# Kernel tuning notes

Measured on AMD Instinct MI355X. Metric: run time of the kernel, lower is better.

Reference implementation:

```python
import jax, jax.numpy as jnp
import numpy as np

DIM = 256
HEADS = 4


def setup_inputs() -> dict:
    key = jax.random.key(0)
    k1, k2, k3, k4, k5 = jax.random.split(key, 5)
    x = jax.random.normal(k1, (8, DIM, 128, 128), dtype=jnp.float32)
    s_in = 1.0 / np.sqrt(DIM)
    Wqkv = jax.random.normal(k2, (DIM, 3 * DIM), dtype=jnp.float32) * s_in
    bqkv = jax.random.normal(k3, (3 * DIM,), dtype=jnp.float32) * 0.02
    Wproj = jax.random.normal(k4, (DIM, DIM), dtype=jnp.float32) * s_in
    bproj = jax.random.normal(k5, (DIM,), dtype=jnp.float32) * 0.02
    return {"x": x, "Wqkv": Wqkv, "bqkv": bqkv, "Wproj": Wproj, "bproj": bproj}


def reference(x, Wqkv, bqkv, Wproj, bproj):
    b, c, h, w = x.shape
    hd = c // HEADS  # head dim
    scale = hd ** -0.5
    # axis='h': (b c h w) -> (b*w, h, c)
    x_r = jnp.transpose(x, (0, 3, 2, 1)).reshape(b * w, h, c)
    qkv = x_r @ Wqkv + bqkv                              # [B, S, 3c]
    qkv = qkv.reshape(b * w, h, 3, HEADS, hd)
    qkv = jnp.transpose(qkv, (2, 0, 3, 1, 4))            # [3, B, H, S, d]
    q, k, v = qkv[0], qkv[1], qkv[2]
    attn = jax.nn.softmax(jnp.einsum('bhqd,bhkd->bhqk', q, k) * scale, axis=-1)
    out = jnp.einsum('bhqk,bhkd->bhqd', attn, v)         # [B, H, S, d]
    out = jnp.transpose(out, (0, 2, 1, 3)).reshape(b * w, h, c)
    out = out @ Wproj + bproj
    # (b*w, h, c) -> (b, c, h, w)
    out = out.reshape(b, w, h, c)
    return jnp.transpose(out, (0, 3, 2, 1))
```

## Files before the change

kernel.cpp:

```cpp
#include <hip/hip_runtime.h>


typedef _Float16 h4 __attribute__((ext_vector_type(4)));
typedef _Float16 h8 __attribute__((ext_vector_type(8)));
typedef float f4 __attribute__((ext_vector_type(4)));
typedef unsigned int u4 __attribute__((ext_vector_type(4)));

#define MFMA32(a, b, c) __builtin_amdgcn_mfma_f32_16x16x32_f16((a), (b), (c), 0, 0, 0)

__device__ __forceinline__ void gll16(const _Float16* g, _Float16* l) {
  __builtin_amdgcn_global_load_lds(
      (const __attribute__((address_space(1))) void*)g,
      (__attribute__((address_space(3))) void*)l, 16, 0, 0);
}

__global__ __launch_bounds__(256) void prep_w(const float* __restrict__ Wqkv,
                                              const float* __restrict__ Wproj,
                                              _Float16* __restrict__ wqt,
                                              _Float16* __restrict__ wpt) {
  int i = blockIdx.x * 256 + threadIdx.x;
  if (i < 768 * 256) {
    int f = i >> 8, c = i & 255;
    wqt[i] = (_Float16)Wqkv[c * 768 + f];
  } else {
    int j = i - 768 * 256;
    int f = j >> 8, c = j & 255;
    wpt[j] = (_Float16)Wproj[c * 256 + f];
  }
}

__global__ __launch_bounds__(256, 4) void k1f(const float* __restrict__ x,
                                              const _Float16* __restrict__ wqt,
                                              const float* __restrict__ bqkv,
                                              _Float16* __restrict__ qkv,
                                              int b_base, int nb) {
  const int wg = blockIdx.x;
  const int xcd = wg & 7, seq = wg >> 3;
  const int id = xcd * (nb * 32) + seq;
  const int hb = id & 127;
  const int rest = id >> 7;
  const int wh = rest & 1, bl = rest >> 1;
  const int b = b_base + bl;
  const int w0 = wh * 64;

  const int tid = threadIdx.x;
  const int lane = tid & 63, wv = tid >> 6;
  const int g = lane >> 4, l16 = lane & 15;
  const int wr = wv >> 1, wc = wv & 1;

  __shared__ __align__(16) char smem[34816];
  _Float16* sXT = (_Float16*)smem;
  _Float16* sA = (_Float16*)smem;
  _Float16* sO = (_Float16*)(smem + 16384);

  {
    const int j0 = tid & 7, r8 = tid >> 3;
#pragma unroll
    for (int p = 0; p < 8; ++p) {
      const int c = p * 32 + r8;
      const float* src = x + (((long)b * 256 + c) * 128 + hb) * 128 + w0;
      f4 v0 = *(const f4*)(src + j0 * 4);
      f4 v1 = *(const f4*)(src + (j0 + 8) * 4);
#pragma unroll
      for (int i = 0; i < 4; ++i) {
        sXT[(j0 * 4 + i) * 264 + c] = (_Float16)v0[i];
        sXT[((j0 + 8) * 4 + i) * 264 + c] = (_Float16)v1[i];
      }
    }
  }
  __syncthreads();

  h8 bfr[4][2][2];
#pragma unroll
  for (int kc = 0; kc < 4; ++kc)
#pragma unroll
    for (int ks = 0; ks < 2; ++ks)
#pragma unroll
      for (int nt = 0; nt < 2; ++nt) {
        const int t = wc * 32 + nt * 16 + l16;
        bfr[kc][ks][nt] =
            *(const h8*)(sXT + t * 264 + kc * 64 + ks * 32 + 8 * g);
      }
  __syncthreads();

  const int r0 = wv * 32;
  const int rl = lane >> 3;
  const int chs = ((lane & 7) ^ rl) * 8;
  const int wl = tid >> 2, dc = tid & 3;
  const int kx = (l16 & 7) * 8;

  for (int ft = 0; ft < 6; ++ft) {
    const int f0 = ft * 128;
    f4 acc[4][2];
#pragma unroll
    for (int mt = 0; mt < 4; ++mt)
#pragma unroll
      for (int nt = 0; nt < 2; ++nt)
#pragma unroll
        for (int r = 0; r < 4; ++r) acc[mt][nt][r] = 0.f;

    for (int kc = 0; kc < 4; ++kc) {
#pragma unroll
      for (int i = 0; i < 4; ++i) {
        const int row = r0 + i * 8 + rl;
        gll16(wqt + (long)(f0 + row) * 256 + kc * 64 + chs, sA + (r0 + i * 8) * 64);
      }
      __syncthreads();
#pragma unroll
      for (int ks = 0; ks < 2; ++ks) {
        const int kk = (ks * 32 + 8 * g) ^ kx;
        h8 af[4];
#pragma unroll
        for (int mt = 0; mt < 4; ++mt)
          af[mt] = *(const h8*)(sA + (wr * 64 + mt * 16 + l16) * 64 + kk);
#pragma unroll
        for (int mt = 0; mt < 4; ++mt)
#pragma unroll
          for (int nt = 0; nt < 2; ++nt)
            acc[mt][nt] = MFMA32(af[mt], bfr[kc][ks][nt], acc[mt][nt]);
      }
      __syncthreads();
    }

#pragma unroll
    for (int mt = 0; mt < 4; ++mt) {
      f4 bb = *(const f4*)(bqkv + f0 + wr * 64 + mt * 16 + 4 * g);
#pragma unroll
      for (int nt = 0; nt < 2; ++nt) {
        const int tl = wc * 32 + nt * 16 + l16;
#pragma unroll
        for (int r = 0; r < 4; ++r)
          sO[tl * 136 + wr * 64 + mt * 16 + 4 * g + r] =
              (_Float16)(acc[mt][nt][r] + bb[r]);
      }
    }
    __syncthreads();
#pragma unroll
    for (int h2 = 0; h2 < 2; ++h2) {
      const int fh = f0 + h2 * 64;
      const int qi = fh >> 8, head = (fh >> 6) & 3;
      _Float16* dst = qkv + (((long)(qi * nb + bl) * 4 + head) * 128 + hb) * 8192 +
                      (w0 + wl) * 64 + dc * 16;
      const _Float16* s = sO + wl * 136 + h2 * 64 + dc * 16;
      *(u4*)dst = *(const u4*)s;
      *(u4*)(dst + 8) = *(const u4*)(s + 8);
    }
    __syncthreads();
  }
}

__global__ __launch_bounds__(256) void k2_attn(const _Float16* __restrict__ qkv,
                                               _Float16* __restrict__ attnout,
                                               int nb) {
  const int w = blockIdx.x, head = blockIdx.y, bl = blockIdx.z;
  const int tid = threadIdx.x;
  const int lane = tid & 63, wv = tid >> 6;
  const int g = lane >> 4, l16 = lane & 15;

  __shared__ __align__(16) char smem[(128 * 72 * 2 + 64 * 136) * 2];
  _Float16* sQ = (_Float16*)smem;
  _Float16* sK = sQ + 128 * 72;
  _Float16* sVT = sK + 128 * 72;
  _Float16* sP = sQ;
  _Float16* sO = sQ;

  const long base = (((long)bl * 4 + head) * 128) * 8192 + (long)w * 64;
  const long QS = (long)nb * 4 * 128 * 8192;
  const _Float16* qg = qkv + base;
  const _Float16* kg = qkv + base + QS;
  const _Float16* vg = qkv + base + 2 * QS;

#pragma unroll
  for (int i = 0; i < 4; ++i) {
    int u = tid + 256 * i;
    int hh = u >> 3, dq = u & 7;
    *(u4*)(sQ + hh * 72 + dq * 8) = *(const u4*)(qg + (long)hh * 8192 + dq * 8);
    *(u4*)(sK + hh * 72 + dq * 8) = *(const u4*)(kg + (long)hh * 8192 + dq * 8);
  }
  {
    const int hh = tid & 127, dcv = tid >> 7;
#pragma unroll
    for (int jj = 0; jj < 4; ++jj) {
      u4 vv = *(const u4*)(vg + (long)hh * 8192 + dcv * 32 + jj * 8);
      const _Float16* pe = (const _Float16*)&vv;
#pragma unroll
      for (int e = 0; e < 8; ++e)
        sVT[(dcv * 32 + jj * 8 + e) * 136 + hh] = pe[e];
    }
  }
  __syncthreads();

  f4 accS[8][2];
  for (int i = 0; i < 8; ++i)
    for (int jt = 0; jt < 2; ++jt)
      for (int r = 0; r < 4; ++r) accS[i][jt][r] = 0.f;
#pragma unroll
  for (int ks = 0; ks < 2; ++ks) {
    const int k = ks * 32 + 8 * g;
    h8 af[8], bf[2];
#pragma unroll
    for (int i = 0; i < 8; ++i)
      af[i] = *(const h8*)(sK + (i * 16 + l16) * 72 + k);
#pragma unroll
    for (int jt = 0; jt < 2; ++jt)
      bf[jt] = *(const h8*)(sQ + (wv * 32 + jt * 16 + l16) * 72 + k);
#pragma unroll
    for (int i = 0; i < 8; ++i)
#pragma unroll
      for (int jt = 0; jt < 2; ++jt)
        accS[i][jt] = MFMA32(af[i], bf[jt], accS[i][jt]);
  }

  float rinv[2];
#pragma unroll
  for (int jt = 0; jt < 2; ++jt) {
    float m = -1e30f;
    for (int i = 0; i < 8; ++i)
      for (int r = 0; r < 4; ++r) m = fmaxf(m, accS[i][jt][r]);
    m = fmaxf(m, __shfl_xor(m, 16));
    m = fmaxf(m, __shfl_xor(m, 32));
    float s = 0.f;
    for (int i = 0; i < 8; ++i)
      for (int r = 0; r < 4; ++r) {
        float p = __expf((accS[i][jt][r] - m) * 0.125f);
        accS[i][jt][r] = p;
        s += p;
      }
    s += __shfl_xor(s, 16);
    s += __shfl_xor(s, 32);
    rinv[jt] = 1.0f / s;
  }

  __syncthreads();
#pragma unroll
  for (int jt = 0; jt < 2; ++jt) {
    const int hq = wv * 32 + jt * 16 + l16;
#pragma unroll
    for (int i = 0; i < 8; ++i) {
      h4 pv;
      pv[0] = (_Float16)accS[i][jt][0];
      pv[1] = (_Float16)accS[i][jt][1];
      pv[2] = (_Float16)accS[i][jt][2];
      pv[3] = (_Float16)accS[i][jt][3];
      *(h4*)(sP + hq * 136 + i * 16 + 4 * g) = pv;
    }
  }
  __syncthreads();

  f4 accO[4][2];
  for (int mt = 0; mt < 4; ++mt)
    for (int jt = 0; jt < 2; ++jt)
      for (int r = 0; r < 4; ++r) accO[mt][jt][r] = 0.f;
#pragma unroll
  for (int i2 = 0; i2 < 4; ++i2) {
    const int k = i2 * 32 + 8 * g;
    h8 av[4], pb[2];
#pragma unroll
    for (int mt = 0; mt < 4; ++mt)
      av[mt] = *(const h8*)(sVT + (mt * 16 + l16) * 136 + k);
#pragma unroll
    for (int jt = 0; jt < 2; ++jt)
      pb[jt] = *(const h8*)(sP + (wv * 32 + jt * 16 + l16) * 136 + k);
#pragma unroll
    for (int mt = 0; mt < 4; ++mt)
#pragma unroll
      for (int jt = 0; jt < 2; ++jt)
        accO[mt][jt] = MFMA32(av[mt], pb[jt], accO[mt][jt]);
  }

  __syncthreads();
#pragma unroll
  for (int mt = 0; mt < 4; ++mt)
#pragma unroll
    for (int jt = 0; jt < 2; ++jt)
#pragma unroll
      for (int r = 0; r < 4; ++r)
        sO[(wv * 32 + jt * 16 + l16) * 72 + mt * 16 + 4 * g + r] =
            (_Float16)(accO[mt][jt][r] * rinv[jt]);
  __syncthreads();

  const int hh = tid >> 1, d0 = (tid & 1) * 32;
  const _Float16* s = sO + hh * 72 + d0;
  _Float16* dst = attnout + ((long)bl * 16384 + hh * 128 + w) * 256 + head * 64 + d0;
#pragma unroll
  for (int e = 0; e < 4; ++e)
    *(u4*)(dst + e * 8) = *(const u4*)(s + e * 8);
}

__global__ __launch_bounds__(256, 4) void k3_proj(const _Float16* __restrict__ attnout,
                                                  const _Float16* __restrict__ wpt,
                                                  const float* __restrict__ bproj,
                                                  float* __restrict__ out,
                                                  int b_base, int nb) {
  const int ct = blockIdx.x, tt = blockIdx.y, bl = blockIdx.z;
  const int b = b_base + bl;
  const int tid = threadIdx.x;
  const int lane = tid & 63, wv = tid >> 6;
  const int g = lane >> 4, l16 = lane & 15;
  const int wr = wv >> 1, wc = wv & 1;
  const int co0 = ct * 128;
  const long t0 = (long)tt * 128;

  __shared__ __align__(16) char smem[33792];
  _Float16* sA = (_Float16*)smem;
  _Float16* sB = sA + 128 * 64;
  float* sOut = (float*)smem;

  f4 acc[4][4];
#pragma unroll
  for (int mt = 0; mt < 4; ++mt)
#pragma unroll
    for (int nt = 0; nt < 4; ++nt)
#pragma unroll
      for (int r = 0; r < 4; ++r) acc[mt][nt][r] = 0.f;

  const _Float16* Ab = wpt + (long)co0 * 256;
  const _Float16* Bb = attnout + ((long)bl * 16384 + t0) * 256;
  const int r0 = wv * 32;
  const int rl = lane >> 3;
  const int chs = ((lane & 7) ^ rl) * 8;
  const int kx = (l16 & 7) * 8;

  for (int kc = 0; kc < 4; ++kc) {
    const int c0 = kc * 64;
#pragma unroll
    for (int i = 0; i < 4; ++i) {
      const int row = r0 + i * 8 + rl;
      gll16(Ab + (long)row * 256 + c0 + chs, sA + (r0 + i * 8) * 64);
      gll16(Bb + (long)row * 256 + c0 + chs, sB + (r0 + i * 8) * 64);
    }
    __syncthreads();
#pragma unroll
    for (int ks = 0; ks < 2; ++ks) {
      const int kk = (ks * 32 + 8 * g) ^ kx;
      h8 af[4], bf[4];
#pragma unroll
      for (int mt = 0; mt < 4; ++mt)
        af[mt] = *(const h8*)(sA + (wr * 64 + mt * 16 + l16) * 64 + kk);
#pragma unroll
      for (int nt = 0; nt < 4; ++nt)
        bf[nt] = *(const h8*)(sB + (wc * 64 + nt * 16 + l16) * 64 + kk);
#pragma unroll
      for (int mt = 0; mt < 4; ++mt)
#pragma unroll
        for (int nt = 0; nt < 4; ++nt)
          acc[mt][nt] = MFMA32(af[mt], bf[nt], acc[mt][nt]);
    }
    __syncthreads();
  }

#pragma unroll
  for (int h2 = 0; h2 < 2; ++h2) {
    if (h2) __syncthreads();
    if (wr == h2) {
#pragma unroll
      for (int mt = 0; mt < 4; ++mt) {
        f4 bb = *(const f4*)(bproj + co0 + h2 * 64 + mt * 16 + 4 * g);
#pragma unroll
        for (int nt = 0; nt < 4; ++nt)
#pragma unroll
          for (int r = 0; r < 4; ++r)
            sOut[(mt * 16 + 4 * g + r) * 132 + wc * 64 + nt * 16 + l16] =
                acc[mt][nt][r] + bb[r];
      }
    }
    __syncthreads();
    const int row = tid >> 2, seg = (tid & 3) * 32;
    const float* s = sOut + row * 132 + seg;
    float* dst = out + ((long)b * 256 + co0 + h2 * 64 + row) * 16384 + t0 + seg;
#pragma unroll
    for (int e = 0; e < 8; ++e)
      *(f4*)(dst + e * 4) = *(const f4*)(s + e * 4);
  }
}

extern "C" void kernel_launch(void* const* d_in, const int* in_sizes, int n_in,
                              void* d_out, int out_size, void* d_ws, size_t ws_size,
                              hipStream_t stream) {
  const float* x = (const float*)d_in[0];
  const float* Wqkv = (const float*)d_in[1];
  const float* bqkv = (const float*)d_in[2];
  const float* Wproj = (const float*)d_in[3];
  const float* bproj = (const float*)d_in[4];
  float* out = (float*)d_out;

  char* ws = (char*)d_ws;
  const long WQT = 393216L, WPT = 131072L;
  const long PER_B = 25165824L + 8388608L;
  long nb_l = ((long)ws_size - (WQT + WPT)) / PER_B;
  int nb = nb_l < 1 ? 1 : (nb_l > 8 ? 8 : (int)nb_l);

  _Float16* wqt = (_Float16*)ws;
  _Float16* wpt = (_Float16*)(ws + WQT);
  _Float16* qkv = (_Float16*)(ws + WQT + WPT);
  _Float16* attnout = (_Float16*)(ws + WQT + WPT + (long)nb * 25165824L);

  prep_w<<<1024, 256, 0, stream>>>(Wqkv, Wproj, wqt, wpt);

  for (int b0 = 0; b0 < 8; b0 += nb) {
    int nbv = (8 - b0 < nb) ? (8 - b0) : nb;
    k1f<<<nbv * 256, 256, 0, stream>>>(x, wqt, bqkv, qkv, b0, nbv);
    k2_attn<<<dim3(128, 4, nbv), 256, 0, stream>>>(qkv, attnout, nbv);
    k3_proj<<<dim3(2, 128, nbv), 256, 0, stream>>>(attnout, wpt, bproj, out, b0, nbv);
  }
}
```

Baseline: 244.2 us.

## Widen QKV projection tile to full 128-column row per block

Each k1f block now handles all 128 w-positions of one (batch, h) row instead of half, so the grid halves and every block does twice the work. The 128x256 weight slice for each feature tile is loaded into LDS once per tile with an XOR swizzle, replacing the four per-k-chunk loads and their barriers. Each wave now covers 128 features by 32 tokens, which reuses each loaded weight fragment across more tokens. The cost is twice the LDS, more accumulator registers and lower occupancy (launch bound 2 instead of 4), and a weight-load phase that no longer overlaps compute.

```diff
diff --git a/kernel.cpp b/kernel.cpp
--- a/kernel.cpp
+++ b/kernel.cpp
@@ -29,42 +29,39 @@
   }
 }
 
-__global__ __launch_bounds__(256, 4) void k1f(const float* __restrict__ x,
+__global__ __launch_bounds__(256, 2) void k1f(const float* __restrict__ x,
                                               const _Float16* __restrict__ wqt,
                                               const float* __restrict__ bqkv,
                                               _Float16* __restrict__ qkv,
                                               int b_base, int nb) {
   const int wg = blockIdx.x;
   const int xcd = wg & 7, seq = wg >> 3;
-  const int id = xcd * (nb * 32) + seq;
+  const int id = xcd * (nb * 16) + seq;
   const int hb = id & 127;
-  const int rest = id >> 7;
-  const int wh = rest & 1, bl = rest >> 1;
+  const int bl = id >> 7;
   const int b = b_base + bl;
-  const int w0 = wh * 64;
 
   const int tid = threadIdx.x;
   const int lane = tid & 63, wv = tid >> 6;
   const int g = lane >> 4, l16 = lane & 15;
-  const int wr = wv >> 1, wc = wv & 1;
-
-  __shared__ __align__(16) char smem[34816];
+
+  __shared__ __align__(16) char smem[67584];
   _Float16* sXT = (_Float16*)smem;
   _Float16* sA = (_Float16*)smem;
-  _Float16* sO = (_Float16*)(smem + 16384);
+  _Float16* sO = (_Float16*)smem;
 
   {
-    const int j0 = tid & 7, r8 = tid >> 3;
-#pragma unroll
-    for (int p = 0; p < 8; ++p) {
-      const int c = p * 32 + r8;
-      const float* src = x + (((long)b * 256 + c) * 128 + hb) * 128 + w0;
+    const int j0 = tid & 15, r16 = tid >> 4;
+#pragma unroll
+    for (int p = 0; p < 16; ++p) {
+      const int c = p * 16 + r16;
+      const float* src = x + (((long)b * 256 + c) * 128 + hb) * 128;
       f4 v0 = *(const f4*)(src + j0 * 4);
-      f4 v1 = *(const f4*)(src + (j0 + 8) * 4);
+      f4 v1 = *(const f4*)(src + (j0 + 16) * 4);
 #pragma unroll
       for (int i = 0; i < 4; ++i) {
         sXT[(j0 * 4 + i) * 264 + c] = (_Float16)v0[i];
-        sXT[((j0 + 8) * 4 + i) * 264 + c] = (_Float16)v1[i];
+        sXT[((j0 + 16) * 4 + i) * 264 + c] = (_Float16)v1[i];
       }
     }
   }
@@ -77,61 +74,62 @@
     for (int ks = 0; ks < 2; ++ks)
 #pragma unroll
       for (int nt = 0; nt < 2; ++nt) {
-        const int t = wc * 32 + nt * 16 + l16;
+        const int t = wv * 32 + nt * 16 + l16;
         bfr[kc][ks][nt] =
             *(const h8*)(sXT + t * 264 + kc * 64 + ks * 32 + 8 * g);
       }
   __syncthreads();
 
-  const int r0 = wv * 32;
-  const int rl = lane >> 3;
-  const int chs = ((lane & 7) ^ rl) * 8;
-  const int wl = tid >> 2, dc = tid & 3;
-  const int kx = (l16 & 7) * 8;
+  const int srow2 = wv * 32;
+  const int c5 = lane & 31, r2 = lane >> 5;
+  const int wl = tid >> 1, dhs = (tid & 1) * 32;
 
   for (int ft = 0; ft < 6; ++ft) {
     const int f0 = ft * 128;
-    f4 acc[4][2];
-#pragma unroll
-    for (int mt = 0; mt < 4; ++mt)
+    f4 acc[8][2];
+#pragma unroll
+    for (int mt = 0; mt < 8; ++mt)
 #pragma unroll
       for (int nt = 0; nt < 2; ++nt)
 #pragma unroll
         for (int r = 0; r < 4; ++r) acc[mt][nt][r] = 0.f;
 
-    for (int kc = 0; kc < 4; ++kc) {
-#pragma unroll
-      for (int i = 0; i < 4; ++i) {
-        const int row = r0 + i * 8 + rl;
-        gll16(wqt + (long)(f0 + row) * 256 + kc * 64 + chs, sA + (r0 + i * 8) * 64);
-      }
-      __syncthreads();
+#pragma unroll
+    for (int i = 0; i < 16; ++i) {
+      const int row = srow2 + i * 2 + r2;
+      const int sch = c5 ^ (row & 7);
+      gll16(wqt + (long)(f0 + row) * 256 + sch * 8, sA + (srow2 + i * 2) * 256);
+    }
+    __syncthreads();
+
+#pragma unroll
+    for (int kc = 0; kc < 4; ++kc)
 #pragma unroll
       for (int ks = 0; ks < 2; ++ks) {
-        const int kk = (ks * 32 + 8 * g) ^ kx;
-        h8 af[4];
-#pragma unroll
-        for (int mt = 0; mt < 4; ++mt)
-          af[mt] = *(const h8*)(sA + (wr * 64 + mt * 16 + l16) * 64 + kk);
-#pragma unroll
-        for (int mt = 0; mt < 4; ++mt)
+        h8 af[8];
+#pragma unroll
+        for (int mt = 0; mt < 8; ++mt) {
+          const int row = mt * 16 + l16;
+          const int q = (kc * 8 + ks * 4 + g) ^ (l16 & 7);
+          af[mt] = *(const h8*)(sA + row * 256 + q * 8);
+        }
+#pragma unroll
+        for (int mt = 0; mt < 8; ++mt)
 #pragma unroll
           for (int nt = 0; nt < 2; ++nt)
             acc[mt][nt] = MFMA32(af[mt], bfr[kc][ks][nt], acc[mt][nt]);
       }
-      __syncthreads();
-    }
-
-#pragma unroll
-    for (int mt = 0; mt < 4; ++mt) {
-      f4 bb = *(const f4*)(bqkv + f0 + wr * 64 + mt * 16 + 4 * g);
+    __syncthreads();
+
+#pragma unroll
+    for (int mt = 0; mt < 8; ++mt) {
+      f4 bb = *(const f4*)(bqkv + f0 + mt * 16 + 4 * g);
 #pragma unroll
       for (int nt = 0; nt < 2; ++nt) {
-        const int tl = wc * 32 + nt * 16 + l16;
+        const int tl = wv * 32 + nt * 16 + l16;
 #pragma unroll
         for (int r = 0; r < 4; ++r)
-          sO[tl * 136 + wr * 64 + mt * 16 + 4 * g + r] =
-              (_Float16)(acc[mt][nt][r] + bb[r]);
+          sO[tl * 136 + mt * 16 + 4 * g + r] = (_Float16)(acc[mt][nt][r] + bb[r]);
       }
     }
     __syncthreads();
@@ -140,10 +138,11 @@
       const int fh = f0 + h2 * 64;
       const int qi = fh >> 8, head = (fh >> 6) & 3;
       _Float16* dst = qkv + (((long)(qi * nb + bl) * 4 + head) * 128 + hb) * 8192 +
-                      (w0 + wl) * 64 + dc * 16;
-      const _Float16* s = sO + wl * 136 + h2 * 64 + dc * 16;
-      *(u4*)dst = *(const u4*)s;
-      *(u4*)(dst + 8) = *(const u4*)(s + 8);
+                      wl * 64 + dhs;
+      const _Float16* s = sO + wl * 136 + h2 * 64 + dhs;
+#pragma unroll
+      for (int e = 0; e < 4; ++e)
+        *(u4*)(dst + e * 8) = *(const u4*)(s + e * 8);
     }
     __syncthreads();
   }
@@ -399,7 +398,7 @@
 
   for (int b0 = 0; b0 < 8; b0 += nb) {
     int nbv = (8 - b0 < nb) ? (8 - b0) : nb;
-    k1f<<<nbv * 256, 256, 0, stream>>>(x, wqt, bqkv, qkv, b0, nbv);
+    k1f<<<nbv * 128, 256, 0, stream>>>(x, wqt, bqkv, qkv, b0, nbv);
     k2_attn<<<dim3(128, 4, nbv), 256, 0, stream>>>(qkv, attnout, nbv);
     k3_proj<<<dim3(2, 128, nbv), 256, 0, stream>>>(attnout, wpt, bproj, out, b0, nbv);
   }
```

Result: no change. 245.8 us (+0.7%).
